# Kernel optimization log

Measured on AMD Instinct MI355X. Metric: run time of the kernel, lower is better.

The kernel has to match this reference:

```python
import jax, jax.numpy as jnp
import numpy as np

N, NX, NQ, NU = 262144, 64, 64, 16
STD = 0.5


def setup_inputs() -> dict:
    key = jax.random.key(0)
    ks = jax.random.split(key, 8)
    x = jax.random.normal(ks[0], (N, NX), jnp.float32)
    u = jax.random.normal(ks[1], (N, NU), jnp.float32)
    A = jax.random.normal(ks[2], (NX, NX), jnp.float32) * STD
    B1 = jax.random.normal(ks[3], (NX, NQ), jnp.float32) * STD
    B2 = jax.random.normal(ks[4], (NX, NU), jnp.float32) * STD
    C1 = jax.random.normal(ks[5], (NQ, NX), jnp.float32) * STD
    # D11 is strictly lower triangular (forward substitution / triangular solve)
    D11 = jnp.tril(jax.random.normal(ks[6], (NQ, NQ), jnp.float32) * STD, -1)
    D12 = jax.random.normal(ks[7], (NQ, NU), jnp.float32) * STD
    bv = jnp.zeros((NQ,), jnp.float32)  # bias=False in original module
    bx = jnp.zeros((NX,), jnp.float32)
    return {"x": x, "u": u, "A": A, "B1": B1, "B2": B2,
            "C1": C1, "D11": D11, "D12": D12, "bv": bv, "bx": bx}


def _calculate_w(x, u, C1, D11, D12, bv):
    """Solve w = act(C1 x + D11 w + D12 u + bv) by forward substitution.
    D11 is strictly lower triangular, so row i of w only depends on rows < i."""
    act = jax.nn.relu
    nq = D11.shape[0]
    base = x @ C1.T + u @ D12.T + bv          # (N, nq): input-dependent part
    eye = jnp.eye(nq, dtype=x.dtype)           # one-hot rows for the scatter

    def step(w, inp):
        d_row, b_col, e = inp                  # (nq,), (N,), (nq,)
        v = b_col + w @ d_row                  # (N,)  uses only already-filled w cols
        w = w + act(v)[:, None] * e            # write column i (matches torch select_w)
        return w, None

    w0 = jnp.zeros((x.shape[0], nq), x.dtype)
    w, _ = jax.lax.scan(step, w0, (D11, base.T, eye))
    return w


def reference(x, u, A, B1, B2, C1, D11, D12, bv, bx):
    # x_dot = A x + B1 w + B2 u + bx
    w = _calculate_w(x, u, C1, D11, D12, bv)
    x_dot = x @ A.T + w @ B1.T + u @ B2.T + bx
    return x_dot
```

## Files before the change

kernel.cpp:

```cpp
#include <hip/hip_runtime.h>
#include <utility>

#define NROWS 262144
#define BT 512
#define RPB 256

typedef float f16v __attribute__((ext_vector_type(16)));
typedef float f4v  __attribute__((ext_vector_type(4)));
typedef float f2v  __attribute__((ext_vector_type(2)));

struct r8 { f2v p[8]; };


__global__ void prep_kernel(const float* __restrict__ A, const float* __restrict__ B1,
                            const float* __restrict__ B2, const float* __restrict__ C1,
                            const float* __restrict__ D11, const float* __restrict__ D12,
                            const float* __restrict__ bv, const float* __restrict__ bx,
                            float* __restrict__ ws) {
    int g = blockIdx.x * 256 + threadIdx.x;
    if (g < 4096) {
        int r = g >> 6, c = g & 63;
        int to = c * 64 + r;
        ws[0     + to] = C1[g];
        ws[4096  + to] = D11[g];
        ws[9280  + to] = A[g];
        ws[13376 + to] = B1[g];
    }
    if (g < 1024) {
        int r = g >> 4, c = g & 15;
        int to = c * 64 + r;
        ws[8192  + to] = D12[g];
        ws[17472 + to] = B2[g];
    }
    if (g < 64) {
        ws[9216  + g] = bv[g];
        ws[18496 + g] = bx[g];
    }
}

__device__ __forceinline__ f16v lds16(const float* p) { return *(const f16v*)p; }
__device__ __forceinline__ r8  lds16p(const float* p) {
    return __builtin_bit_cast(r8, *(const f16v*)p);
}

__device__ __forceinline__ void fence_sched() { __builtin_amdgcn_sched_barrier(0); }

template<int Q>
__device__ __forceinline__ float qbcast(float v) {
    return __int_as_float(__builtin_amdgcn_update_dpp(
        0, __float_as_int(v), Q * 0x55, 0xF, 0xF, true));
}

__device__ __forceinline__ void pkfma8(r8& a, const f16v m, const float s) {
    const r8 mp = __builtin_bit_cast(r8, m);
    f2v ss; ss[0] = s; ss[1] = s;
#pragma unroll
    for (int k = 0; k < 8; k++)
        asm("v_pk_fma_f32 %0, %1, %2, %0" : "+v"(a.p[k]) : "v"(mp.p[k]), "v"(ss));
}

__device__ __forceinline__ void relu8(r8& a) {
#pragma unroll
    for (int k = 0; k < 8; k++) {
        a.p[k][0] = fmaxf(a.p[k][0], 0.0f);
        a.p[k][1] = fmaxf(a.p[k][1], 0.0f);
    }
}

template<int E>
__device__ __forceinline__ float getel(const r8& a) { return a.p[E >> 1][E & 1]; }

template<int I>
__device__ __forceinline__ void substep2(r8& s0, r8& s1, const float* D11s, int c16) {
    const float w0 = fmaxf(qbcast<(I >> 4)>(getel<(I & 15)>(s0)), 0.0f);
    const float w1 = fmaxf(qbcast<(I >> 4)>(getel<(I & 15)>(s1)), 0.0f);
    const f16v m = lds16(D11s + I * 64 + c16);
    pkfma8(s0, m, w0);
    pkfma8(s1, m, w1);
}
template<int... Is>
__device__ __forceinline__ void subst_all2(r8& s0, r8& s1, const float* D11s,
                                           int c16, std::integer_sequence<int, Is...>) {
    (substep2<Is>(s0, s1, D11s, c16), ...);
}

template<int J>
__device__ __forceinline__ void mv64step2(r8& a0, r8& a1, const float* Ms,
                                          int c16, const r8& f0, const r8& f1) {
    const f16v m = lds16(Ms + J * 64 + c16);
    pkfma8(a0, m, qbcast<(J >> 4)>(getel<(J & 15)>(f0)));
    pkfma8(a1, m, qbcast<(J >> 4)>(getel<(J & 15)>(f1)));
}
template<int... Js>
__device__ __forceinline__ void mv64_2(r8& a0, r8& a1, const float* Ms, int c16,
                                       const r8& f0, const r8& f1,
                                       std::integer_sequence<int, Js...>) {
    (mv64step2<Js>(a0, a1, Ms, c16, f0, f1), ...);
}

template<int J>
__device__ __forceinline__ void mv16step2(r8& a0, r8& a1, const float* Ms,
                                          int c16, const f4v& f0, const f4v& f1) {
    const f16v m = lds16(Ms + J * 64 + c16);
    pkfma8(a0, m, qbcast<(J >> 2)>(f0[J & 3]));
    pkfma8(a1, m, qbcast<(J >> 2)>(f1[J & 3]));
}
template<int... Js>
__device__ __forceinline__ void mv16_2(r8& a0, r8& a1, const float* Ms, int c16,
                                       const f4v& f0, const f4v& f1,
                                       std::integer_sequence<int, Js...>) {
    (mv16step2<Js>(a0, a1, Ms, c16, f0, f1), ...);
}

__global__ __launch_bounds__(BT, 4) void renl2_fused(const float* __restrict__ x,
                                                     const float* __restrict__ u,
                                                     const float* __restrict__ ws,
                                                     float* __restrict__ out) {
    __shared__ __align__(64) float sm[9280];
    const int tid = threadIdx.x;
    const int c16 = (tid & 3) << 4;
    const size_t row0 = (size_t)blockIdx.x * RPB;

    const r8  xf0 = lds16p(x + row0 * 64 + (size_t)tid * 16);
    const r8  xf1 = lds16p(x + (row0 + 128) * 64 + (size_t)tid * 16);
    const f4v uf0 = *(const f4v*)(u + row0 * 16 + (size_t)tid * 4);
    const f4v uf1 = *(const f4v*)(u + (row0 + 128) * 16 + (size_t)tid * 4);

    const float4* wsv = (const float4*)ws;
    float4* smv = (float4*)sm;
#pragma unroll
    for (int i = 0; i < 4; i++) smv[tid + i * BT] = wsv[tid + i * BT];
    if (tid < 2320 - 4 * BT) smv[tid + 4 * BT] = wsv[tid + 4 * BT];
    __syncthreads();

    r8 s0 = lds16p(sm + 9216 + c16);
    r8 s1 = s0;
    mv64_2(s0, s1, sm + 0,    c16, xf0, xf1, std::make_integer_sequence<int, 64>{});
    mv16_2(s0, s1, sm + 8192, c16, uf0, uf1, std::make_integer_sequence<int, 16>{});
    fence_sched();

    subst_all2(s0, s1, sm + 4096, c16, std::make_integer_sequence<int, 64>{});
    relu8(s0);
    relu8(s1);
    fence_sched();

    __syncthreads();
#pragma unroll
    for (int i = 0; i < 4; i++) smv[tid + i * BT] = wsv[2320 + tid + i * BT];
    if (tid < 2320 - 4 * BT) smv[tid + 4 * BT] = wsv[2320 + tid + 4 * BT];
    __syncthreads();

    r8 acc0 = lds16p(sm + 9216 + c16);
    r8 acc1 = acc0;
    mv64_2(acc0, acc1, sm + 4096, c16, s0, s1, std::make_integer_sequence<int, 64>{});
    fence_sched();

    size_t r0 = row0;
    asm volatile("" : "+s"(r0));
    const r8  xg0 = lds16p(x + r0 * 64 + (size_t)tid * 16);
    const r8  xg1 = lds16p(x + (r0 + 128) * 64 + (size_t)tid * 16);
    const f4v ug0 = *(const f4v*)(u + r0 * 16 + (size_t)tid * 4);
    const f4v ug1 = *(const f4v*)(u + (r0 + 128) * 16 + (size_t)tid * 4);
    mv64_2(acc0, acc1, sm + 0,    c16, xg0, xg1, std::make_integer_sequence<int, 64>{});
    mv16_2(acc0, acc1, sm + 8192, c16, ug0, ug1, std::make_integer_sequence<int, 16>{});

    const size_t q = (size_t)(tid >> 2);
    *(f16v*)(out + (row0 + q) * 64 + c16)       = __builtin_bit_cast(f16v, acc0);
    *(f16v*)(out + (row0 + 128 + q) * 64 + c16) = __builtin_bit_cast(f16v, acc1);
}

extern "C" void kernel_launch(void* const* d_in, const int* in_sizes, int n_in,
                              void* d_out, int out_size, void* d_ws, size_t ws_size,
                              hipStream_t stream) {
    const float* x   = (const float*)d_in[0];
    const float* u   = (const float*)d_in[1];
    const float* A   = (const float*)d_in[2];
    const float* B1  = (const float*)d_in[3];
    const float* B2  = (const float*)d_in[4];
    const float* C1  = (const float*)d_in[5];
    const float* D11 = (const float*)d_in[6];
    const float* D12 = (const float*)d_in[7];
    const float* bv  = (const float*)d_in[8];
    const float* bx  = (const float*)d_in[9];
    float* out = (float*)d_out;
    float* ws  = (float*)d_ws;

    prep_kernel<<<16, 256, 0, stream>>>(A, B1, B2, C1, D11, D12, bv, bx, ws);
    renl2_fused<<<NROWS / RPB, BT, 0, stream>>>(x, u, ws, out);
}
```

Before: 242.2 us.

## Split weight reads between LDS and global loads, drop packed FMA asm

In the dense matrix-vector stages, each 16-wide weight chunk is now read as 12 floats from LDS plus 4 floats straight from the global workspace. The intent is to take some pressure off LDS bandwidth by sending part of the traffic through the vector memory/L1 path. The inline v_pk_fma_f32 asm is replaced with plain float4 multiply-add that the compiler schedules itself. Launch bounds drop from 4 to 3 blocks per CU, allowing more registers at the cost of occupancy. The extra global loads inside the unrolled loops add latency that may not be hidden.

After: 312.8 us. +29.2%, slower.

```diff
diff --git a/kernel.cpp b/kernel.cpp
--- a/kernel.cpp
+++ b/kernel.cpp
@@ -7,9 +7,8 @@
 
 typedef float f16v __attribute__((ext_vector_type(16)));
 typedef float f4v  __attribute__((ext_vector_type(4)));
-typedef float f2v  __attribute__((ext_vector_type(2)));
-
-struct r8 { f2v p[8]; };
+
+struct qch { f4v q[4]; };
 
 
 __global__ void prep_kernel(const float* __restrict__ A, const float* __restrict__ B1,
@@ -38,9 +37,21 @@
     }
 }
 
-__device__ __forceinline__ f16v lds16(const float* p) { return *(const f16v*)p; }
-__device__ __forceinline__ r8  lds16p(const float* p) {
-    return __builtin_bit_cast(r8, *(const f16v*)p);
+__device__ __forceinline__ qch ldsq16(const float* p) {
+    qch r;
+    r.q[0] = *(const f4v*)(p);
+    r.q[1] = *(const f4v*)(p + 4);
+    r.q[2] = *(const f4v*)(p + 8);
+    r.q[3] = *(const f4v*)(p + 12);
+    return r;
+}
+__device__ __forceinline__ qch mix12_4(const float* lp, const float* gp) {
+    qch r;
+    r.q[0] = *(const f4v*)(lp);
+    r.q[1] = *(const f4v*)(lp + 4);
+    r.q[2] = *(const f4v*)(lp + 8);
+    r.q[3] = *(const f4v*)(gp);
+    return r;
 }
 
 __device__ __forceinline__ void fence_sched() { __builtin_amdgcn_sched_barrier(0); }
@@ -51,68 +62,68 @@
         0, __float_as_int(v), Q * 0x55, 0xF, 0xF, true));
 }
 
-__device__ __forceinline__ void pkfma8(r8& a, const f16v m, const float s) {
-    const r8 mp = __builtin_bit_cast(r8, m);
-    f2v ss; ss[0] = s; ss[1] = s;
-#pragma unroll
-    for (int k = 0; k < 8; k++)
-        asm("v_pk_fma_f32 %0, %1, %2, %0" : "+v"(a.p[k]) : "v"(mp.p[k]), "v"(ss));
-}
-
-__device__ __forceinline__ void relu8(r8& a) {
-#pragma unroll
-    for (int k = 0; k < 8; k++) {
-        a.p[k][0] = fmaxf(a.p[k][0], 0.0f);
-        a.p[k][1] = fmaxf(a.p[k][1], 0.0f);
-    }
+__device__ __forceinline__ void fma4(qch& a, const qch& m, const float s) {
+#pragma unroll
+    for (int k = 0; k < 4; k++) a.q[k] += m.q[k] * s;
+}
+
+__device__ __forceinline__ void relu16(qch& a) {
+#pragma unroll
+    for (int k = 0; k < 4; k++)
+#pragma unroll
+        for (int e = 0; e < 4; e++) a.q[k][e] = fmaxf(a.q[k][e], 0.0f);
 }
 
 template<int E>
-__device__ __forceinline__ float getel(const r8& a) { return a.p[E >> 1][E & 1]; }
+__device__ __forceinline__ float getel(const qch& a) { return a.q[E >> 2][E & 3]; }
 
 template<int I>
-__device__ __forceinline__ void substep2(r8& s0, r8& s1, const float* D11s, int c16) {
+__device__ __forceinline__ void substep2(qch& s0, qch& s1, const float* D11s, int c16) {
     const float w0 = fmaxf(qbcast<(I >> 4)>(getel<(I & 15)>(s0)), 0.0f);
     const float w1 = fmaxf(qbcast<(I >> 4)>(getel<(I & 15)>(s1)), 0.0f);
-    const f16v m = lds16(D11s + I * 64 + c16);
-    pkfma8(s0, m, w0);
-    pkfma8(s1, m, w1);
+    const qch m = ldsq16(D11s + I * 64 + c16);
+    fma4(s0, m, w0);
+    fma4(s1, m, w1);
 }
 template<int... Is>
-__device__ __forceinline__ void subst_all2(r8& s0, r8& s1, const float* D11s,
+__device__ __forceinline__ void subst_all2(qch& s0, qch& s1, const float* D11s,
                                            int c16, std::integer_sequence<int, Is...>) {
     (substep2<Is>(s0, s1, D11s, c16), ...);
 }
 
 template<int J>
-__device__ __forceinline__ void mv64step2(r8& a0, r8& a1, const float* Ms,
-                                          int c16, const r8& f0, const r8& f1) {
-    const f16v m = lds16(Ms + J * 64 + c16);
-    pkfma8(a0, m, qbcast<(J >> 4)>(getel<(J & 15)>(f0)));
-    pkfma8(a1, m, qbcast<(J >> 4)>(getel<(J & 15)>(f1)));
+__device__ __forceinline__ void mv64step2(qch& a0, qch& a1, const float* Ml,
+                                          const float* Mg, int c16,
+                                          const qch& f0, const qch& f1) {
+    const qch m = mix12_4(Ml + J * 64 + c16, Mg + J * 64 + c16 + 12);
+    fma4(a0, m, qbcast<(J >> 4)>(getel<(J & 15)>(f0)));
+    fma4(a1, m, qbcast<(J >> 4)>(getel<(J & 15)>(f1)));
 }
 template<int... Js>
-__device__ __forceinline__ void mv64_2(r8& a0, r8& a1, const float* Ms, int c16,
-                                       const r8& f0, const r8& f1,
+__device__ __forceinline__ void mv64_2(qch& a0, qch& a1, const float* Ml,
+                                       const float* Mg, int c16,
+                                       const qch& f0, const qch& f1,
                                        std::integer_sequence<int, Js...>) {
-    (mv64step2<Js>(a0, a1, Ms, c16, f0, f1), ...);
+    (mv64step2<Js>(a0, a1, Ml, Mg, c16, f0, f1), ...);
 }
 
 template<int J>
-__device__ __forceinline__ void mv16step2(r8& a0, r8& a1, const float* Ms,
-                                          int c16, const f4v& f0, const f4v& f1) {
-    const f16v m = lds16(Ms + J * 64 + c16);
-    pkfma8(a0, m, qbcast<(J >> 2)>(f0[J & 3]));
-    pkfma8(a1, m, qbcast<(J >> 2)>(f1[J & 3]));
+__device__ __forceinline__ void mv16step2(qch& a0, qch& a1, const float* Ml,
+                                          const float* Mg, int c16,
+                                          const f4v& f0, const f4v& f1) {
+    const qch m = mix12_4(Ml + J * 64 + c16, Mg + J * 64 + c16 + 12);
+    fma4(a0, m, qbcast<(J >> 2)>(f0[J & 3]));
+    fma4(a1, m, qbcast<(J >> 2)>(f1[J & 3]));
 }
 template<int... Js>
-__device__ __forceinline__ void mv16_2(r8& a0, r8& a1, const float* Ms, int c16,
+__device__ __forceinline__ void mv16_2(qch& a0, qch& a1, const float* Ml,
+                                       const float* Mg, int c16,
                                        const f4v& f0, const f4v& f1,
                                        std::integer_sequence<int, Js...>) {
-    (mv16step2<Js>(a0, a1, Ms, c16, f0, f1), ...);
-}
-
-__global__ __launch_bounds__(BT, 4) void renl2_fused(const float* __restrict__ x,
+    (mv16step2<Js>(a0, a1, Ml, Mg, c16, f0, f1), ...);
+}
+
+__global__ __launch_bounds__(BT, 3) void renl2_fused(const float* __restrict__ x,
                                                      const float* __restrict__ u,
                                                      const float* __restrict__ ws,
                                                      float* __restrict__ out) {
@@ -121,8 +132,8 @@
     const int c16 = (tid & 3) << 4;
     const size_t row0 = (size_t)blockIdx.x * RPB;
 
-    const r8  xf0 = lds16p(x + row0 * 64 + (size_t)tid * 16);
-    const r8  xf1 = lds16p(x + (row0 + 128) * 64 + (size_t)tid * 16);
+    const qch xf0 = ldsq16(x + row0 * 64 + (size_t)tid * 16);
+    const qch xf1 = ldsq16(x + (row0 + 128) * 64 + (size_t)tid * 16);
     const f4v uf0 = *(const f4v*)(u + row0 * 16 + (size_t)tid * 4);
     const f4v uf1 = *(const f4v*)(u + (row0 + 128) * 16 + (size_t)tid * 4);
 
@@ -133,15 +144,17 @@
     if (tid < 2320 - 4 * BT) smv[tid + 4 * BT] = wsv[tid + 4 * BT];
     __syncthreads();
 
-    r8 s0 = lds16p(sm + 9216 + c16);
-    r8 s1 = s0;
-    mv64_2(s0, s1, sm + 0,    c16, xf0, xf1, std::make_integer_sequence<int, 64>{});
-    mv16_2(s0, s1, sm + 8192, c16, uf0, uf1, std::make_integer_sequence<int, 16>{});
+    qch s0 = ldsq16(sm + 9216 + c16);
+    qch s1 = s0;
+    mv64_2(s0, s1, sm + 0,    ws + 0,    c16, xf0, xf1,
+           std::make_integer_sequence<int, 64>{});
+    mv16_2(s0, s1, sm + 8192, ws + 8192, c16, uf0, uf1,
+           std::make_integer_sequence<int, 16>{});
     fence_sched();
 
     subst_all2(s0, s1, sm + 4096, c16, std::make_integer_sequence<int, 64>{});
-    relu8(s0);
-    relu8(s1);
+    relu16(s0);
+    relu16(s1);
     fence_sched();
 
     __syncthreads();
@@ -150,19 +163,22 @@
     if (tid < 2320 - 4 * BT) smv[tid + 4 * BT] = wsv[2320 + tid + 4 * BT];
     __syncthreads();
 
-    r8 acc0 = lds16p(sm + 9216 + c16);
-    r8 acc1 = acc0;
-    mv64_2(acc0, acc1, sm + 4096, c16, s0, s1, std::make_integer_sequence<int, 64>{});
+    qch acc0 = ldsq16(sm + 9216 + c16);
+    qch acc1 = acc0;
+    mv64_2(acc0, acc1, sm + 4096, ws + 13376, c16, s0, s1,
+           std::make_integer_sequence<int, 64>{});
     fence_sched();
 
     size_t r0 = row0;
     asm volatile("" : "+s"(r0));
-    const r8  xg0 = lds16p(x + r0 * 64 + (size_t)tid * 16);
-    const r8  xg1 = lds16p(x + (r0 + 128) * 64 + (size_t)tid * 16);
+    const qch xg0 = ldsq16(x + r0 * 64 + (size_t)tid * 16);
+    const qch xg1 = ldsq16(x + (r0 + 128) * 64 + (size_t)tid * 16);
     const f4v ug0 = *(const f4v*)(u + r0 * 16 + (size_t)tid * 4);
     const f4v ug1 = *(const f4v*)(u + (r0 + 128) * 16 + (size_t)tid * 4);
-    mv64_2(acc0, acc1, sm + 0,    c16, xg0, xg1, std::make_integer_sequence<int, 64>{});
-    mv16_2(acc0, acc1, sm + 8192, c16, ug0, ug1, std::make_integer_sequence<int, 16>{});
+    mv64_2(acc0, acc1, sm + 0,    ws + 9280,  c16, xg0, xg1,
+           std::make_integer_sequence<int, 64>{});
+    mv16_2(acc0, acc1, sm + 8192, ws + 17472, c16, ug0, ug1,
+           std::make_integer_sequence<int, 16>{});
 
     const size_t q = (size_t)(tid >> 2);
     *(f16v*)(out + (row0 + q) * 64 + c16)       = __builtin_bit_cast(f16v, acc0);
```
